# Kernel tuning notes

Hardware: AMD Instinct MI355X
Metric: run time of the kernel (lower is better)

## Reference

```python
import jax, jax.numpy as jnp
import numpy as np

N = 100000      # nodes
F_IN = 512      # input features
H = 128         # hidden
C = 16          # classes
E = 3200000     # edges
K = 10          # propagation hops (lg_k == gg_k == 10)
ALPHA = 0.1


def ppr_temp(K, alpha):
    t = alpha * (1.0 - alpha) ** np.arange(K + 1)
    t[-1] = (1.0 - alpha) ** K
    return jnp.asarray(t, dtype=jnp.float32)


def setup_inputs() -> dict:
    key = jax.random.key(0)
    ks = jax.random.split(key, 8)
    x = jax.random.normal(ks[0], (N, F_IN), dtype=jnp.float32)
    edge_index = jax.random.randint(ks[1], (2, E), 0, N, dtype=jnp.int64)
    # Local branch: kaiming-uniform-ish linears
    W1_l = jax.random.uniform(ks[2], (F_IN, H), jnp.float32, -1.0, 1.0) * np.sqrt(6.0 / F_IN)
    b1_l = jnp.zeros((H,), jnp.float32)
    W2_l = jax.random.uniform(ks[3], (H, C), jnp.float32, -1.0, 1.0) * np.sqrt(6.0 / H)
    b2_l = jnp.zeros((C,), jnp.float32)
    temp_l = ppr_temp(K, ALPHA)
    # Global branch: uniform(-0.1, 0.1) linears
    W1_g = jax.random.uniform(ks[4], (F_IN, H), jnp.float32, -0.1, 0.1)
    b1_g = jnp.zeros((H,), jnp.float32)
    W2_g = jax.random.uniform(ks[5], (H, C), jnp.float32, -0.1, 0.1)
    b2_g = jnp.zeros((C,), jnp.float32)
    temp_g = ppr_temp(K, ALPHA)
    return {"x": x, "edge_index": edge_index,
            "W1_l": W1_l, "b1_l": b1_l, "W2_l": W2_l, "b2_l": b2_l, "temp_l": temp_l,
            "W1_g": W1_g, "b1_g": b1_g, "W2_g": W2_g, "b2_g": b2_g, "temp_g": temp_g}


def gpr_prop(x, edge_index, temp):
    # gcn_norm: add self-loops with weight 1, symmetric normalization
    row = jnp.concatenate([edge_index[0], jnp.arange(N, dtype=edge_index.dtype)])
    col = jnp.concatenate([edge_index[1], jnp.arange(N, dtype=edge_index.dtype)])
    deg = jax.ops.segment_sum(jnp.ones(row.shape[0], x.dtype), col, num_segments=N)
    dis = jnp.where(deg > 0, jax.lax.rsqrt(deg), 0.0).astype(x.dtype)
    norm = dis[row] * dis[col]  # [E+N]

    def step(carry, gamma):
        xc, hid = carry
        # gather-scale-scatter: out[col] += norm * xc[row]
        xn = jax.ops.segment_sum(norm[:, None] * xc[row], col, num_segments=N)
        return (xn, hid + gamma * xn), None

    (_, hidden), _ = jax.lax.scan(step, (x, x * temp[0]), temp[1:])
    return hidden


def gprgnn_branch(x, edge_index, W1, b1, W2, b2, temp):
    h1 = jax.nn.relu(x @ W1 + b1)          # [N, H]
    h2 = h1 @ W2 + b2                      # [N, C]
    h2 = gpr_prop(h2, edge_index, temp)    # K-hop GPR diffusion
    return h1, h2, jax.nn.log_softmax(h2, axis=1)


def reference(x, edge_index, W1_l, b1_l, W2_l, b2_l, temp_l,
              W1_g, b1_g, W2_g, b2_g, temp_g):
    h1_l, h2_l, prob_l = gprgnn_branch(x, edge_index, W1_l, b1_l, W2_l, b2_l, temp_l)
    h1_g, h2_g, prob_g = gprgnn_branch(x, edge_index, W1_g, b1_g, W2_g, b2_g, temp_g)
    return (h1_l, h2_l, prob_l, h1_g, h2_g, prob_g)
```

## Files before the change

### kernel.cpp

```cpp
#include <hip/hip_runtime.h>
#include <stdint.h>

#define F_IN 512
#define HDIM 128
#define CDIM 16
#define KHOPS 10

#define NBMAX 1024
#define CSTR 16
#define CHUNK 8192
#define CH2 32768

typedef __bf16 bf16x8 __attribute__((ext_vector_type(8)));
typedef float f32x4 __attribute__((ext_vector_type(4)));

typedef __attribute__((address_space(3))) unsigned int lds_uint;
typedef const __attribute__((address_space(1))) unsigned int g_uint;

__device__ __forceinline__ void dma16(const void* g, void* l) {
    __builtin_amdgcn_global_load_lds((g_uint*)g, (lds_uint*)l, 16, 0, 0);
}

__device__ __forceinline__ unsigned short f2bf(float f) {
    unsigned int u = __float_as_uint(f);
    u += 0x7FFFu + ((u >> 16) & 1u);
    return (unsigned short)(u >> 16);
}

__device__ __forceinline__ bf16x8 ld_bf8(const unsigned short* p) {
    uint4 u = *reinterpret_cast<const uint4*>(p);
    return __builtin_bit_cast(bf16x8, u);
}


__global__ __launch_bounds__(256) void k_ccount(const int* __restrict__ eidx,
                                                int* __restrict__ ccnt, int E) {
    __shared__ int lh[NBMAX];
    int t = threadIdx.x;
    int base = blockIdx.x * CH2;
    int lim = E - base; if (lim > CH2) lim = CH2;
    for (int i = t; i < NBMAX; i += 256) lh[i] = 0;
    __syncthreads();
    for (int j = t; j < lim; j += 256)
        atomicAdd(&lh[eidx[(size_t)E + base + j] >> 8], 1);
    __syncthreads();
    for (int i = t; i < NBMAX; i += 256) {
        int v = lh[i];
        if (v) atomicAdd(&ccnt[i], v);
    }
}

__global__ void k_cscan(const int* __restrict__ ccnt, int* __restrict__ coffs,
                        int* __restrict__ ccur, int nbuk) {
    __shared__ int sh[256];
    int t = threadIdx.x;
    int i0 = t * 4;
    int v0 = ccnt[i0 + 0], v1 = ccnt[i0 + 1], v2 = ccnt[i0 + 2], v3 = ccnt[i0 + 3];
    int s = v0 + v1 + v2 + v3;
    sh[t] = s;
    __syncthreads();
    for (int d = 1; d < 256; d <<= 1) {
        int x = (t >= d) ? sh[t - d] : 0;
        __syncthreads();
        sh[t] += x;
        __syncthreads();
    }
    int e0 = sh[t] - s;
    int e1 = e0 + v0, e2 = e1 + v1, e3 = e2 + v2;
    coffs[i0 + 0] = e0;
    coffs[i0 + 1] = e1;
    coffs[i0 + 2] = e2;
    coffs[i0 + 3] = e3;
    if (t == 255) coffs[1024] = e3 + v3;
    if (i0 + 0 < nbuk) ccur[(i0 + 0) * CSTR] = e0;
    if (i0 + 1 < nbuk) ccur[(i0 + 1) * CSTR] = e1;
    if (i0 + 2 < nbuk) ccur[(i0 + 2) * CSTR] = e2;
    if (i0 + 3 < nbuk) ccur[(i0 + 3) * CSTR] = e3;
}

__global__ __launch_bounds__(256) void k_part(
    const int* __restrict__ eidx, int* __restrict__ ccur,
    uint2* __restrict__ cedges, int E)
{
    __shared__ int lh[NBMAX];
    __shared__ int loff[NBMAX];
    __shared__ int lcur[NBMAX];
    __shared__ int gbase[NBMAX];
    __shared__ int sh[256];

    int t = threadIdx.x;
    int base = blockIdx.x * CHUNK;
    int lim = E - base; if (lim > CHUNK) lim = CHUNK;

    for (int i = t; i < NBMAX; i += 256) lh[i] = 0;
    __syncthreads();

    for (int j = t; j < lim; j += 256) {
        int c = eidx[(size_t)E + base + j];
        atomicAdd(&lh[c >> 8], 1);
    }
    __syncthreads();

    int i0 = t * 4;
    int v0 = lh[i0 + 0], v1 = lh[i0 + 1], v2 = lh[i0 + 2], v3 = lh[i0 + 3];
    int s = v0 + v1 + v2 + v3;
    sh[t] = s;
    __syncthreads();
    for (int d = 1; d < 256; d <<= 1) {
        int x = (t >= d) ? sh[t - d] : 0;
        __syncthreads();
        sh[t] += x;
        __syncthreads();
    }
    int excl = sh[t] - s;
    loff[i0 + 0] = excl; lcur[i0 + 0] = excl;
    gbase[i0 + 0] = v0 ? atomicAdd(&ccur[(i0 + 0) * CSTR], v0) : 0;
    excl += v0;
    loff[i0 + 1] = excl; lcur[i0 + 1] = excl;
    gbase[i0 + 1] = v1 ? atomicAdd(&ccur[(i0 + 1) * CSTR], v1) : 0;
    excl += v1;
    loff[i0 + 2] = excl; lcur[i0 + 2] = excl;
    gbase[i0 + 2] = v2 ? atomicAdd(&ccur[(i0 + 2) * CSTR], v2) : 0;
    excl += v2;
    loff[i0 + 3] = excl; lcur[i0 + 3] = excl;
    gbase[i0 + 3] = v3 ? atomicAdd(&ccur[(i0 + 3) * CSTR], v3) : 0;
    __syncthreads();

    for (int j = t; j < lim; j += 256) {
        int r = eidx[base + j];
        int c = eidx[(size_t)E + base + j];
        int b = c >> 8;
        int lp = atomicAdd(&lcur[b], 1);
        int gpos = gbase[b] + (lp - loff[b]);
        uint2 u; u.x = (unsigned)r; u.y = (unsigned)c;
        cedges[gpos] = u;
    }
}

__global__ __launch_bounds__(256) void k_fineA(
    const uint2* __restrict__ cedges, const int* __restrict__ coffs,
    int* __restrict__ cnt, float* __restrict__ dis, int* __restrict__ offs, int N)
{
    __shared__ int lh[256];
    __shared__ int sh[256];
    int b = blockIdx.x;
    int t = threadIdx.x;
    int col0 = b << 8;
    int segs = coffs[b];
    int sege = coffs[b + 1];
    lh[t] = 0;
    __syncthreads();
    for (int j = segs + t; j < sege; j += 256)
        atomicAdd(&lh[(int)cedges[j].y - col0], 1);
    __syncthreads();
    int c = lh[t];
    sh[t] = c;
    __syncthreads();
    for (int d = 1; d < 256; d <<= 1) {
        int x = (t >= d) ? sh[t - d] : 0;
        __syncthreads();
        sh[t] += x;
        __syncthreads();
    }
    int excl = sh[t] - c;
    int col = col0 + t;
    if (col < N) {
        cnt[col] = c;
        dis[col] = rsqrtf((float)(c + 1));
        offs[col] = segs + excl;
    }
}

__global__ __launch_bounds__(256) void k_fineB(
    const uint2* __restrict__ cedges, const int* __restrict__ coffs,
    const int* __restrict__ offs, const float* __restrict__ dis,
    uint2* __restrict__ srcnrm, int N)
{
    __shared__ int lcur[256];
    __shared__ float ldis[256];
    int b = blockIdx.x;
    int col0 = b << 8;
    int t = threadIdx.x;
    int col = col0 + t;
    int segs = coffs[b];
    int sege = coffs[b + 1];
    if (col < N) { lcur[t] = offs[col]; ldis[t] = dis[col]; }
    __syncthreads();
    for (int j = segs + t; j < sege; j += 256) {
        uint2 e = cedges[j];
        int li = (int)e.y - col0;
        int pos = atomicAdd(&lcur[li], 1);
        uint2 u;
        u.x = e.x;
        u.y = __float_as_uint(dis[e.x] * ldis[li]);
        srcnrm[pos] = u;
    }
}


__global__ void k_xbf(const float* __restrict__ x, unsigned short* __restrict__ xbf) {
    size_t i = (size_t)blockIdx.x * 2048 + (size_t)threadIdx.x * 8;
    float4 a = *reinterpret_cast<const float4*>(&x[i]);
    float4 b = *reinterpret_cast<const float4*>(&x[i + 4]);
    unsigned short s[8];
    s[0] = f2bf(a.x); s[1] = f2bf(a.y); s[2] = f2bf(a.z); s[3] = f2bf(a.w);
    s[4] = f2bf(b.x); s[5] = f2bf(b.y); s[6] = f2bf(b.z); s[7] = f2bf(b.w);
    *reinterpret_cast<uint4*>(&xbf[i]) = *reinterpret_cast<uint4*>(s);
}


__global__ void k_w1t(const float* __restrict__ W1l, const float* __restrict__ W1g,
                      unsigned short* __restrict__ W1Tl, unsigned short* __restrict__ W1Tg) {
    const float* W1 = blockIdx.y ? W1g : W1l;
    unsigned short* W1T = blockIdx.y ? W1Tg : W1Tl;
    int idx = blockIdx.x * 256 + threadIdx.x;
    int n = idx >> 6;
    int k0 = (idx & 63) * 8;
    unsigned short tmp[8];
    for (int j = 0; j < 8; j++)
        tmp[j] = f2bf(W1[(size_t)(k0 + j) * HDIM + n]);
    *reinterpret_cast<uint4*>(&W1T[(size_t)n * F_IN + k0]) = *reinterpret_cast<uint4*>(tmp);
}


__global__ __launch_bounds__(256, 4) void k_gemm(
    const unsigned short* __restrict__ xbf,
    const unsigned short* __restrict__ W1Tl, const float* __restrict__ b1l,
    const float* __restrict__ W2l, const float* __restrict__ b2l, const float* __restrict__ tl,
    const unsigned short* __restrict__ W1Tg, const float* __restrict__ b1g,
    const float* __restrict__ W2g, const float* __restrict__ b2g, const float* __restrict__ tg,
    float* __restrict__ h1l, float* __restrict__ h1g,
    float* __restrict__ xc0, float* __restrict__ hid, int nNode)
{
    const int br = blockIdx.y;
    const unsigned short* w1t = br ? W1Tg : W1Tl;
    const float* B1 = br ? b1g : b1l;
    const float* W2 = br ? W2g : W2l;
    const float* B2 = br ? b2g : b2l;
    const float* tp = br ? tg : tl;
    float* h1 = br ? h1g : h1l;

    __shared__ __align__(16) unsigned short sm[17408];
    unsigned short* As = sm;
    unsigned short* Bs = sm + 8192;
    unsigned short* Hs = sm;

    const int t = threadIdx.x;
    const int lane = t & 63;
    const int w = t >> 6;
    const int row0 = blockIdx.x * 128;

    f32x4 acc[2][8];
    for (int i = 0; i < 2; i++)
        for (int j = 0; j < 8; j++)
            acc[i][j] = f32x4{0.f, 0.f, 0.f, 0.f};

    const int m16 = lane & 15;
    const int q = lane >> 4;

    for (int k0 = 0; k0 < F_IN; k0 += 64) {
        #pragma unroll
        for (int j = 0; j < 4; j++) {
            int S0 = w * 256 + j * 64;
            int S = S0 + lane;
            int row = S >> 3;
            int cb = (S & 7) ^ (row & 7);
            dma16(&xbf[(size_t)(row0 + row) * F_IN + k0 + cb * 8], &As[(size_t)S0 * 8]);
        }
        #pragma unroll
        for (int j = 0; j < 4; j++) {
            int S0 = w * 256 + j * 64;
            int S = S0 + lane;
            int n = S >> 3;
            int cb = (S & 7) ^ (n & 7);
            dma16(&w1t[(size_t)n * F_IN + k0 + cb * 8], &Bs[(size_t)S0 * 8]);
        }
        __syncthreads();

        #pragma unroll
        for (int ksub = 0; ksub < 2; ksub++) {
            bf16x8 bf[8];
            #pragma unroll
            for (int ns = 0; ns < 8; ns++) {
                int n = ns * 16 + m16;
                int slot = n * 8 + ((ksub * 4 + q) ^ (n & 7));
                bf[ns] = ld_bf8(&Bs[slot * 8]);
            }
            bf16x8 af[2];
            #pragma unroll
            for (int ms = 0; ms < 2; ms++) {
                int row = w * 32 + ms * 16 + m16;
                int slot = row * 8 + ((ksub * 4 + q) ^ (row & 7));
                af[ms] = ld_bf8(&As[slot * 8]);
            }
            #pragma unroll
            for (int ns = 0; ns < 8; ns++)
                #pragma unroll
                for (int ms = 0; ms < 2; ms++)
                    acc[ms][ns] = __builtin_amdgcn_mfma_f32_16x16x32_bf16(af[ms], bf[ns], acc[ms][ns], 0, 0, 0);
        }
        __syncthreads();
    }

    #pragma unroll
    for (int ms = 0; ms < 2; ms++) {
        #pragma unroll
        for (int ns = 0; ns < 8; ns++) {
            int n = ns * 16 + m16;
            float bias = B1[n];
            #pragma unroll
            for (int r = 0; r < 4; r++) {
                int m = w * 32 + ms * 16 + q * 4 + r;
                float v = acc[ms][ns][r] + bias;
                v = v > 0.f ? v : 0.f;
                Hs[m * 136 + n] = f2bf(v);
                int node = row0 + m;
                if (node < nNode) h1[(size_t)node * HDIM + n] = v;
            }
        }
    }
    __syncthreads();

    {
        float t0 = tp[0];
        float bias = B2[m16];
        #pragma unroll
        for (int mi = 0; mi < 2; mi++) {
            int mt = w * 2 + mi;
            f32x4 acc2 = f32x4{bias, bias, bias, bias};
            #pragma unroll
            for (int kb = 0; kb < 4; kb++) {
                bf16x8 hf = ld_bf8(&Hs[(mt * 16 + m16) * 136 + kb * 32 + q * 8]);
                unsigned short wtmp[8];
                #pragma unroll
                for (int j = 0; j < 8; j++)
                    wtmp[j] = f2bf(W2[(size_t)(kb * 32 + q * 8 + j) * CDIM + m16]);
                bf16x8 wf = ld_bf8(wtmp);
                acc2 = __builtin_amdgcn_mfma_f32_16x16x32_bf16(hf, wf, acc2, 0, 0, 0);
            }
            #pragma unroll
            for (int r = 0; r < 4; r++) {
                int node = row0 + mt * 16 + q * 4 + r;
                if (node < nNode) {
                    size_t idx = (size_t)node * 32 + (size_t)br * 16 + m16;
                    xc0[idx] = acc2[r];
                    hid[idx] = t0 * acc2[r];
                }
            }
        }
    }
}


__global__ __launch_bounds__(256) void k_hop(
    const float* __restrict__ xin, float* __restrict__ xout,
    float* __restrict__ hid, const uint2* __restrict__ srcnrm,
    const int* __restrict__ offs, const int* __restrict__ cnt,
    const float* __restrict__ dis,
    const float* __restrict__ tl, const float* __restrict__ tg,
    int hop, int N)
{
    int t = threadIdx.x;
    int v = blockIdx.x * 32 + (t >> 3);
    int c4 = (t & 7) * 4;
    if (v >= N) return;
    int off = offs[v];
    int m = cnt[v];
    float d = dis[v];
    size_t vbase = (size_t)v * 32 + c4;
    float4 xv = *reinterpret_cast<const float4*>(xin + vbase);
    float dd = d * d;
    float4 acc = make_float4(dd * xv.x, dd * xv.y, dd * xv.z, dd * xv.w);
    const uint2* ep = srcnrm + off;
    int i = 0;
    for (; i + 8 <= m; i += 8) {
        uint2 u[8];
        #pragma unroll
        for (int j = 0; j < 8; j++) u[j] = ep[i + j];
        float4 xs[8];
        #pragma unroll
        for (int j = 0; j < 8; j++)
            xs[j] = *reinterpret_cast<const float4*>(xin + (size_t)u[j].x * 32 + c4);
        #pragma unroll
        for (int j = 0; j < 8; j++) {
            float nrm = __uint_as_float(u[j].y);
            acc.x = fmaf(nrm, xs[j].x, acc.x);
            acc.y = fmaf(nrm, xs[j].y, acc.y);
            acc.z = fmaf(nrm, xs[j].z, acc.z);
            acc.w = fmaf(nrm, xs[j].w, acc.w);
        }
    }
    for (; i < m; i++) {
        uint2 u = ep[i];
        float nrm = __uint_as_float(u.y);
        float4 xs = *reinterpret_cast<const float4*>(xin + (size_t)u.x * 32 + c4);
        acc.x = fmaf(nrm, xs.x, acc.x);
        acc.y = fmaf(nrm, xs.y, acc.y);
        acc.z = fmaf(nrm, xs.z, acc.z);
        acc.w = fmaf(nrm, xs.w, acc.w);
    }
    *reinterpret_cast<float4*>(xout + vbase) = acc;
    float gamma = (c4 < 16 ? tl : tg)[hop];
    float4 h = *reinterpret_cast<const float4*>(hid + vbase);
    h.x = fmaf(gamma, acc.x, h.x);
    h.y = fmaf(gamma, acc.y, h.y);
    h.z = fmaf(gamma, acc.z, h.z);
    h.w = fmaf(gamma, acc.w, h.w);
    *reinterpret_cast<float4*>(hid + vbase) = h;
}


__global__ void k_final(const float* __restrict__ hid,
                        float* __restrict__ h2l, float* __restrict__ pl,
                        float* __restrict__ h2g, float* __restrict__ pg, int N)
{
    int t = threadIdx.x;
    int v = blockIdx.x * 128 + (t >> 1);
    int br = t & 1;
    if (v >= N) return;
    float xv[16];
    const float* src = &hid[(size_t)v * 32 + (size_t)br * 16];
    for (int j = 0; j < 16; j += 4)
        *reinterpret_cast<float4*>(&xv[j]) = *reinterpret_cast<const float4*>(&src[j]);
    float mx = xv[0];
    for (int j = 1; j < 16; j++) mx = fmaxf(mx, xv[j]);
    float s = 0.f;
    for (int j = 0; j < 16; j++) s += __expf(xv[j] - mx);
    float lse = mx + __logf(s);
    float* h2 = br ? h2g : h2l;
    float* pp = br ? pg : pl;
    for (int j = 0; j < 16; j++) {
        h2[(size_t)v * 16 + j] = xv[j];
        pp[(size_t)v * 16 + j] = xv[j] - lse;
    }
}


extern "C" void kernel_launch(void* const* d_in, const int* in_sizes, int n_in,
                              void* d_out, int out_size, void* d_ws, size_t ws_size,
                              hipStream_t stream)
{
    const float* x   = (const float*)d_in[0];
    const int*   eidx= (const int*)d_in[1];
    const float* W1l = (const float*)d_in[2];
    const float* b1l = (const float*)d_in[3];
    const float* W2l = (const float*)d_in[4];
    const float* b2l = (const float*)d_in[5];
    const float* tl  = (const float*)d_in[6];
    const float* W1g = (const float*)d_in[7];
    const float* b1g = (const float*)d_in[8];
    const float* W2g = (const float*)d_in[9];
    const float* b2g = (const float*)d_in[10];
    const float* tg  = (const float*)d_in[11];

    const int N = in_sizes[0] / F_IN;
    const int E = in_sizes[1] / 2;

    float* out = (float*)d_out;
    float* h1l = out;
    float* h2l = h1l + (size_t)N * HDIM;
    float* pl  = h2l + (size_t)N * CDIM;
    float* h1g = pl  + (size_t)N * CDIM;
    float* h2g = h1g + (size_t)N * HDIM;
    float* pg  = h2g + (size_t)N * CDIM;

    char* ws = (char*)d_ws;
    auto alloc = [&](size_t bytes) -> char* {
        char* p = ws;
        ws += (bytes + 1023) & ~(size_t)1023;
        return p;
    };
    int*   cnt      = (int*)alloc((size_t)N * 4);
    int*   offs     = (int*)alloc((size_t)N * 4);
    int*   ccnt     = (int*)alloc((size_t)(NBMAX + 1) * 4);
    int*   coffs    = (int*)alloc((size_t)(NBMAX + 1) * 4);
    int*   ccur     = (int*)alloc((size_t)NBMAX * CSTR * 4);
    float* dis      = (float*)alloc((size_t)N * 4);
    uint2* srcnrm   = (uint2*)alloc((size_t)E * 8);
    float* xcA      = (float*)alloc((size_t)N * 32 * 4);
    float* xcB      = (float*)alloc((size_t)N * 32 * 4);
    float* hid      = (float*)alloc((size_t)N * 32 * 4);
    unsigned short* W1Tl = (unsigned short*)alloc((size_t)HDIM * F_IN * 2);
    unsigned short* W1Tg = (unsigned short*)alloc((size_t)HDIM * F_IN * 2);
    unsigned short* xbf  = (unsigned short*)alloc((size_t)(N + 256) * F_IN * 2);
    uint2* cedges = (uint2*)xbf;

    hipMemsetAsync(ccnt, 0, (size_t)(NBMAX + 1) * 4, stream);

    int nbuk = (N + 255) / 256;

    k_ccount<<<(E + CH2 - 1) / CH2, 256, 0, stream>>>(eidx, ccnt, E);
    k_cscan<<<1, 256, 0, stream>>>(ccnt, coffs, ccur, nbuk);
    k_part<<<(E + CHUNK - 1) / CHUNK, 256, 0, stream>>>(eidx, ccur, cedges, E);
    k_fineA<<<nbuk, 256, 0, stream>>>(cedges, coffs, cnt, dis, offs, N);
    k_fineB<<<nbuk, 256, 0, stream>>>(cedges, coffs, offs, dis, srcnrm, N);

    k_xbf<<<(int)(((size_t)N * F_IN) / 2048), 256, 0, stream>>>(x, xbf);
    dim3 gw(32, 2);
    k_w1t<<<gw, 256, 0, stream>>>(W1l, W1g, W1Tl, W1Tg);

    dim3 gg((N + 127) / 128, 2);
    k_gemm<<<gg, 256, 0, stream>>>(xbf, W1Tl, b1l, W2l, b2l, tl,
                                   W1Tg, b1g, W2g, b2g, tg,
                                   h1l, h1g, xcA, hid, N);

    int gh = (N + 31) / 32;
    float* a = xcA;
    float* b = xcB;
    for (int k = 1; k <= KHOPS; k++) {
        k_hop<<<gh, 256, 0, stream>>>(a, b, hid, srcnrm, offs, cnt, dis, tl, tg, k, N);
        float* tmp = a; a = b; b = tmp;
    }
    k_final<<<(N + 127) / 128, 256, 0, stream>>>(hid, h2l, pl, h2g, pg, N);
}
```

Before: 1.189 ms.

## Fuse K propagation hops and log-softmax into one persistent kernel with grid barriers

Replaces the ten per-hop launches and the final log-softmax kernel with one persistent kernel of 1024 blocks. Each thread keeps its node slices, the hidden accumulator and the degree data in registers across hops, and a global atomic barrier separates the hops. The edge norm is factored into source and destination scaling, so the edge list shrinks from 8 bytes to 4 bytes per edge and the hidden state is never written to memory. The risks are the correctness of the spin barrier, which needs all blocks co-resident (1024 blocks at 4 per CU), and less latency hiding, since each thread walks up to four node slices one after another.

```diff
diff --git a/kernel.cpp b/kernel.cpp
--- a/kernel.cpp
+++ b/kernel.cpp
@@ -10,6 +10,9 @@
 #define CSTR 16
 #define CHUNK 8192
 #define CH2 32768
+
+#define PROP_BLOCKS 1024
+#define MAXIT 4
 
 typedef __bf16 bf16x8 __attribute__((ext_vector_type(8)));
 typedef float f32x4 __attribute__((ext_vector_type(4)));
@@ -173,27 +176,22 @@
 
 __global__ __launch_bounds__(256) void k_fineB(
     const uint2* __restrict__ cedges, const int* __restrict__ coffs,
-    const int* __restrict__ offs, const float* __restrict__ dis,
-    uint2* __restrict__ srcnrm, int N)
+    const int* __restrict__ offs, int* __restrict__ srcs, int N)
 {
     __shared__ int lcur[256];
-    __shared__ float ldis[256];
     int b = blockIdx.x;
     int col0 = b << 8;
     int t = threadIdx.x;
     int col = col0 + t;
     int segs = coffs[b];
     int sege = coffs[b + 1];
-    if (col < N) { lcur[t] = offs[col]; ldis[t] = dis[col]; }
+    if (col < N) lcur[t] = offs[col];
     __syncthreads();
     for (int j = segs + t; j < sege; j += 256) {
         uint2 e = cedges[j];
         int li = (int)e.y - col0;
         int pos = atomicAdd(&lcur[li], 1);
-        uint2 u;
-        u.x = e.x;
-        u.y = __float_as_uint(dis[e.x] * ldis[li]);
-        srcnrm[pos] = u;
+        srcs[pos] = (int)e.x;
     }
 }
 
@@ -226,18 +224,17 @@
 __global__ __launch_bounds__(256, 4) void k_gemm(
     const unsigned short* __restrict__ xbf,
     const unsigned short* __restrict__ W1Tl, const float* __restrict__ b1l,
-    const float* __restrict__ W2l, const float* __restrict__ b2l, const float* __restrict__ tl,
+    const float* __restrict__ W2l, const float* __restrict__ b2l,
     const unsigned short* __restrict__ W1Tg, const float* __restrict__ b1g,
-    const float* __restrict__ W2g, const float* __restrict__ b2g, const float* __restrict__ tg,
+    const float* __restrict__ W2g, const float* __restrict__ b2g,
     float* __restrict__ h1l, float* __restrict__ h1g,
-    float* __restrict__ xc0, float* __restrict__ hid, int nNode)
+    float* __restrict__ xc0, int nNode)
 {
     const int br = blockIdx.y;
     const unsigned short* w1t = br ? W1Tg : W1Tl;
     const float* B1 = br ? b1g : b1l;
     const float* W2 = br ? W2g : W2l;
     const float* B2 = br ? b2g : b2l;
-    const float* tp = br ? tg : tl;
     float* h1 = br ? h1g : h1l;
 
     __shared__ __align__(16) unsigned short sm[17408];
@@ -322,7 +319,6 @@
     __syncthreads();
 
     {
-        float t0 = tp[0];
         float bias = B2[m16];
         #pragma unroll
         for (int mi = 0; mi < 2; mi++) {
@@ -344,7 +340,6 @@
                 if (node < nNode) {
                     size_t idx = (size_t)node * 32 + (size_t)br * 16 + m16;
                     xc0[idx] = acc2[r];
-                    hid[idx] = t0 * acc2[r];
                 }
             }
         }
@@ -352,86 +347,128 @@
 }
 
 
-__global__ __launch_bounds__(256) void k_hop(
-    const float* __restrict__ xin, float* __restrict__ xout,
-    float* __restrict__ hid, const uint2* __restrict__ srcnrm,
-    const int* __restrict__ offs, const int* __restrict__ cnt,
-    const float* __restrict__ dis,
+__device__ __forceinline__ void gbar(unsigned int* bar, unsigned int tgt) {
+    __threadfence();
+    __syncthreads();
+    if (threadIdx.x == 0) {
+        atomicAdd(bar, 1u);
+        while (atomicAdd(bar, 0u) < tgt) __builtin_amdgcn_s_sleep(2);
+    }
+    __syncthreads();
+    __threadfence();
+}
+
+__global__ __launch_bounds__(256, 4) void k_prop(
+    const float* __restrict__ x0,
+    float* __restrict__ yA, float* __restrict__ yB,
+    const int* __restrict__ srcs, const int* __restrict__ offs,
+    const int* __restrict__ cnt, const float* __restrict__ dis,
     const float* __restrict__ tl, const float* __restrict__ tg,
-    int hop, int N)
+    float* __restrict__ h2l, float* __restrict__ pl,
+    float* __restrict__ h2g, float* __restrict__ pg,
+    unsigned int* __restrict__ bar, int N)
 {
-    int t = threadIdx.x;
-    int v = blockIdx.x * 32 + (t >> 3);
-    int c4 = (t & 7) * 4;
-    if (v >= N) return;
-    int off = offs[v];
-    int m = cnt[v];
-    float d = dis[v];
-    size_t vbase = (size_t)v * 32 + c4;
-    float4 xv = *reinterpret_cast<const float4*>(xin + vbase);
-    float dd = d * d;
-    float4 acc = make_float4(dd * xv.x, dd * xv.y, dd * xv.z, dd * xv.w);
-    const uint2* ep = srcnrm + off;
-    int i = 0;
-    for (; i + 8 <= m; i += 8) {
-        uint2 u[8];
+    const int T = gridDim.x * 256;
+    const int gtid = blockIdx.x * 256 + threadIdx.x;
+    const int NP = N * 8;
+    const int slice = gtid & 7;
+    const int c4 = slice * 4;
+    const float* tp = slice < 4 ? tl : tg;
+
+    float4 cur[MAXIT], hid[MAXIT];
+    int off[MAXIT], deg[MAXIT];
+    float dv[MAXIT];
+
+    const float t0 = tp[0];
+    #pragma unroll
+    for (int it = 0; it < MAXIT; ++it) {
+        int p = it * T + gtid;
+        if (p < NP) {
+            int v = p >> 3;
+            off[it] = offs[v];
+            deg[it] = cnt[v];
+            float d = dis[v];
+            dv[it] = d;
+            float4 xv = *reinterpret_cast<const float4*>(x0 + (size_t)p * 4);
+            cur[it] = make_float4(d * xv.x, d * xv.y, d * xv.z, d * xv.w);
+            hid[it] = make_float4(t0 * xv.x, t0 * xv.y, t0 * xv.z, t0 * xv.w);
+            *reinterpret_cast<float4*>(yA + (size_t)p * 4) = cur[it];
+        } else {
+            off[it] = 0; deg[it] = 0; dv[it] = 0.f;
+            cur[it] = make_float4(0.f, 0.f, 0.f, 0.f);
+            hid[it] = make_float4(0.f, 0.f, 0.f, 0.f);
+        }
+    }
+
+    gbar(bar, gridDim.x);
+
+    const float* yin = yA;
+    float* yout = yB;
+    for (int k = 1; k <= KHOPS; ++k) {
+        float gma = tp[k];
         #pragma unroll
-        for (int j = 0; j < 8; j++) u[j] = ep[i + j];
-        float4 xs[8];
-        #pragma unroll
-        for (int j = 0; j < 8; j++)
-            xs[j] = *reinterpret_cast<const float4*>(xin + (size_t)u[j].x * 32 + c4);
-        #pragma unroll
-        for (int j = 0; j < 8; j++) {
-            float nrm = __uint_as_float(u[j].y);
-            acc.x = fmaf(nrm, xs[j].x, acc.x);
-            acc.y = fmaf(nrm, xs[j].y, acc.y);
-            acc.z = fmaf(nrm, xs[j].z, acc.z);
-            acc.w = fmaf(nrm, xs[j].w, acc.w);
-        }
-    }
-    for (; i < m; i++) {
-        uint2 u = ep[i];
-        float nrm = __uint_as_float(u.y);
-        float4 xs = *reinterpret_cast<const float4*>(xin + (size_t)u.x * 32 + c4);
-        acc.x = fmaf(nrm, xs.x, acc.x);
-        acc.y = fmaf(nrm, xs.y, acc.y);
-        acc.z = fmaf(nrm, xs.z, acc.z);
-        acc.w = fmaf(nrm, xs.w, acc.w);
-    }
-    *reinterpret_cast<float4*>(xout + vbase) = acc;
-    float gamma = (c4 < 16 ? tl : tg)[hop];
-    float4 h = *reinterpret_cast<const float4*>(hid + vbase);
-    h.x = fmaf(gamma, acc.x, h.x);
-    h.y = fmaf(gamma, acc.y, h.y);
-    h.z = fmaf(gamma, acc.z, h.z);
-    h.w = fmaf(gamma, acc.w, h.w);
-    *reinterpret_cast<float4*>(hid + vbase) = h;
-}
-
-
-__global__ void k_final(const float* __restrict__ hid,
-                        float* __restrict__ h2l, float* __restrict__ pl,
-                        float* __restrict__ h2g, float* __restrict__ pg, int N)
-{
-    int t = threadIdx.x;
-    int v = blockIdx.x * 128 + (t >> 1);
-    int br = t & 1;
-    if (v >= N) return;
-    float xv[16];
-    const float* src = &hid[(size_t)v * 32 + (size_t)br * 16];
-    for (int j = 0; j < 16; j += 4)
-        *reinterpret_cast<float4*>(&xv[j]) = *reinterpret_cast<const float4*>(&src[j]);
-    float mx = xv[0];
-    for (int j = 1; j < 16; j++) mx = fmaxf(mx, xv[j]);
-    float s = 0.f;
-    for (int j = 0; j < 16; j++) s += __expf(xv[j] - mx);
-    float lse = mx + __logf(s);
-    float* h2 = br ? h2g : h2l;
-    float* pp = br ? pg : pl;
-    for (int j = 0; j < 16; j++) {
-        h2[(size_t)v * 16 + j] = xv[j];
-        pp[(size_t)v * 16 + j] = xv[j] - lse;
+        for (int it = 0; it < MAXIT; ++it) {
+            int p = it * T + gtid;
+            if (p >= NP) continue;
+            const int* ep = srcs + off[it];
+            int m = deg[it];
+            float4 acc = cur[it];
+            int i = 0;
+            for (; i + 8 <= m; i += 8) {
+                int u[8];
+                #pragma unroll
+                for (int j = 0; j < 8; ++j) u[j] = ep[i + j];
+                float4 xs[8];
+                #pragma unroll
+                for (int j = 0; j < 8; ++j)
+                    xs[j] = *reinterpret_cast<const float4*>(yin + (size_t)u[j] * 32 + c4);
+                #pragma unroll
+                for (int j = 0; j < 8; ++j) {
+                    acc.x += xs[j].x; acc.y += xs[j].y;
+                    acc.z += xs[j].z; acc.w += xs[j].w;
+                }
+            }
+            for (; i < m; ++i) {
+                float4 xs = *reinterpret_cast<const float4*>(yin + (size_t)ep[i] * 32 + c4);
+                acc.x += xs.x; acc.y += xs.y; acc.z += xs.z; acc.w += xs.w;
+            }
+            float d = dv[it];
+            float4 xn = make_float4(d * acc.x, d * acc.y, d * acc.z, d * acc.w);
+            hid[it].x = fmaf(gma, xn.x, hid[it].x);
+            hid[it].y = fmaf(gma, xn.y, hid[it].y);
+            hid[it].z = fmaf(gma, xn.z, hid[it].z);
+            hid[it].w = fmaf(gma, xn.w, hid[it].w);
+            cur[it] = make_float4(d * xn.x, d * xn.y, d * xn.z, d * xn.w);
+            if (k < KHOPS)
+                *reinterpret_cast<float4*>(yout + (size_t)p * 4) = cur[it];
+        }
+        if (k < KHOPS) {
+            gbar(bar, (unsigned)(k + 1) * gridDim.x);
+            const float* tin = yin; yin = yout; yout = (float*)tin;
+        }
+    }
+
+    #pragma unroll
+    for (int it = 0; it < MAXIT; ++it) {
+        int p = it * T + gtid;
+        float4 hv = hid[it];
+        float mloc = fmaxf(fmaxf(hv.x, hv.y), fmaxf(hv.z, hv.w));
+        mloc = fmaxf(mloc, __shfl_xor(mloc, 1));
+        mloc = fmaxf(mloc, __shfl_xor(mloc, 2));
+        float sl = __expf(hv.x - mloc) + __expf(hv.y - mloc) +
+                   __expf(hv.z - mloc) + __expf(hv.w - mloc);
+        sl += __shfl_xor(sl, 1);
+        sl += __shfl_xor(sl, 2);
+        float lse = mloc + __logf(sl);
+        if (p < NP) {
+            int v = p >> 3;
+            int r = (slice & 3) * 4;
+            float* h2 = slice < 4 ? h2l : h2g;
+            float* pp = slice < 4 ? pl : pg;
+            *reinterpret_cast<float4*>(h2 + (size_t)v * 16 + r) = hv;
+            float4 po = make_float4(hv.x - lse, hv.y - lse, hv.z - lse, hv.w - lse);
+            *reinterpret_cast<float4*>(pp + (size_t)v * 16 + r) = po;
+        }
     }
 }
 
@@ -475,17 +512,19 @@
     int*   ccnt     = (int*)alloc((size_t)(NBMAX + 1) * 4);
     int*   coffs    = (int*)alloc((size_t)(NBMAX + 1) * 4);
     int*   ccur     = (int*)alloc((size_t)NBMAX * CSTR * 4);
+    unsigned int* bar = (unsigned int*)alloc(1024);
     float* dis      = (float*)alloc((size_t)N * 4);
-    uint2* srcnrm   = (uint2*)alloc((size_t)E * 8);
+    int*   srcs     = (int*)alloc((size_t)E * 4);
     float* xcA      = (float*)alloc((size_t)N * 32 * 4);
-    float* xcB      = (float*)alloc((size_t)N * 32 * 4);
-    float* hid      = (float*)alloc((size_t)N * 32 * 4);
+    float* yA       = (float*)alloc((size_t)N * 32 * 4);
+    float* yB       = (float*)alloc((size_t)N * 32 * 4);
     unsigned short* W1Tl = (unsigned short*)alloc((size_t)HDIM * F_IN * 2);
     unsigned short* W1Tg = (unsigned short*)alloc((size_t)HDIM * F_IN * 2);
     unsigned short* xbf  = (unsigned short*)alloc((size_t)(N + 256) * F_IN * 2);
     uint2* cedges = (uint2*)xbf;
 
     hipMemsetAsync(ccnt, 0, (size_t)(NBMAX + 1) * 4, stream);
+    hipMemsetAsync(bar, 0, 1024, stream);
 
     int nbuk = (N + 255) / 256;
 
@@ -493,23 +532,17 @@
     k_cscan<<<1, 256, 0, stream>>>(ccnt, coffs, ccur, nbuk);
     k_part<<<(E + CHUNK - 1) / CHUNK, 256, 0, stream>>>(eidx, ccur, cedges, E);
     k_fineA<<<nbuk, 256, 0, stream>>>(cedges, coffs, cnt, dis, offs, N);
-    k_fineB<<<nbuk, 256, 0, stream>>>(cedges, coffs, offs, dis, srcnrm, N);
+    k_fineB<<<nbuk, 256, 0, stream>>>(cedges, coffs, offs, srcs, N);
 
     k_xbf<<<(int)(((size_t)N * F_IN) / 2048), 256, 0, stream>>>(x, xbf);
     dim3 gw(32, 2);
     k_w1t<<<gw, 256, 0, stream>>>(W1l, W1g, W1Tl, W1Tg);
 
     dim3 gg((N + 127) / 128, 2);
-    k_gemm<<<gg, 256, 0, stream>>>(xbf, W1Tl, b1l, W2l, b2l, tl,
-                                   W1Tg, b1g, W2g, b2g, tg,
-                                   h1l, h1g, xcA, hid, N);
-
-    int gh = (N + 31) / 32;
-    float* a = xcA;
-    float* b = xcB;
-    for (int k = 1; k <= KHOPS; k++) {
-        k_hop<<<gh, 256, 0, stream>>>(a, b, hid, srcnrm, offs, cnt, dis, tl, tg, k, N);
-        float* tmp = a; a = b; b = tmp;
-    }
-    k_final<<<(N + 127) / 128, 256, 0, stream>>>(hid, h2l, pl, h2g, pg, N);
-}
+    k_gemm<<<gg, 256, 0, stream>>>(xbf, W1Tl, b1l, W2l, b2l,
+                                   W1Tg, b1g, W2g, b2g,
+                                   h1l, h1g, xcA, N);
+
+    k_prop<<<PROP_BLOCKS, 256, 0, stream>>>(xcA, yA, yB, srcs, offs, cnt, dis,
+                                            tl, tg, h2l, pl, h2g, pg, bar, N);
+}
```

Result: slower. 3.429 ms (+188.5%).

## Fold symmetric norm into prescaled features and split propagation into channel passes

Applied to the files above, without the earlier changes.

Propagation now stores y = D^{-1/2} x, so each hop becomes a plain sum of gathered neighbour rows, scaled by dis[v] on output. This drops the per-edge norm weight and halves the edge array to a single int per edge. Features move to a pass-major layout (8 passes of float4 per node), with one thread per node per pass, so each gather reads a 16-byte row from a compact 1.6MB slab that fits in cache, instead of eight threads sharing a 128-byte row. The trade-off is more index reads, since each edge's source index is now loaded once per pass (eight times per hop).

```diff
diff --git a/kernel.cpp b/kernel.cpp
--- a/kernel.cpp
+++ b/kernel.cpp
@@ -173,27 +173,22 @@
 
 __global__ __launch_bounds__(256) void k_fineB(
     const uint2* __restrict__ cedges, const int* __restrict__ coffs,
-    const int* __restrict__ offs, const float* __restrict__ dis,
-    uint2* __restrict__ srcnrm, int N)
+    const int* __restrict__ offs, int* __restrict__ srcs, int N)
 {
     __shared__ int lcur[256];
-    __shared__ float ldis[256];
     int b = blockIdx.x;
     int col0 = b << 8;
     int t = threadIdx.x;
     int col = col0 + t;
     int segs = coffs[b];
     int sege = coffs[b + 1];
-    if (col < N) { lcur[t] = offs[col]; ldis[t] = dis[col]; }
+    if (col < N) lcur[t] = offs[col];
     __syncthreads();
     for (int j = segs + t; j < sege; j += 256) {
         uint2 e = cedges[j];
         int li = (int)e.y - col0;
         int pos = atomicAdd(&lcur[li], 1);
-        uint2 u;
-        u.x = e.x;
-        u.y = __float_as_uint(dis[e.x] * ldis[li]);
-        srcnrm[pos] = u;
+        srcs[pos] = (int)e.x;
     }
 }
 
@@ -229,8 +224,9 @@
     const float* __restrict__ W2l, const float* __restrict__ b2l, const float* __restrict__ tl,
     const unsigned short* __restrict__ W1Tg, const float* __restrict__ b1g,
     const float* __restrict__ W2g, const float* __restrict__ b2g, const float* __restrict__ tg,
+    const float* __restrict__ dis,
     float* __restrict__ h1l, float* __restrict__ h1g,
-    float* __restrict__ xc0, float* __restrict__ hid, int nNode)
+    float* __restrict__ y0, float* __restrict__ hidb, int nNode)
 {
     const int br = blockIdx.y;
     const unsigned short* w1t = br ? W1Tg : W1Tl;
@@ -324,6 +320,8 @@
     {
         float t0 = tp[0];
         float bias = B2[m16];
+        int pass = br * 4 + (m16 >> 2);
+        int slot = m16 & 3;
         #pragma unroll
         for (int mi = 0; mi < 2; mi++) {
             int mt = w * 2 + mi;
@@ -342,9 +340,10 @@
             for (int r = 0; r < 4; r++) {
                 int node = row0 + mt * 16 + q * 4 + r;
                 if (node < nNode) {
-                    size_t idx = (size_t)node * 32 + (size_t)br * 16 + m16;
-                    xc0[idx] = acc2[r];
-                    hid[idx] = t0 * acc2[r];
+                    size_t idx = ((size_t)pass * nNode + node) * 4 + slot;
+                    float val = acc2[r];
+                    y0[idx] = dis[node] * val;
+                    hidb[idx] = t0 * val;
                 }
             }
         }
@@ -352,65 +351,58 @@
 }
 
 
-__global__ __launch_bounds__(256) void k_hop(
-    const float* __restrict__ xin, float* __restrict__ xout,
-    float* __restrict__ hid, const uint2* __restrict__ srcnrm,
+__global__ __launch_bounds__(256) void k_hop2(
+    const float* __restrict__ yin, float* __restrict__ yout,
+    float* __restrict__ hidb, const int* __restrict__ srcs,
     const int* __restrict__ offs, const int* __restrict__ cnt,
     const float* __restrict__ dis,
     const float* __restrict__ tl, const float* __restrict__ tg,
-    int hop, int N)
-{
-    int t = threadIdx.x;
-    int v = blockIdx.x * 32 + (t >> 3);
-    int c4 = (t & 7) * 4;
+    int hop, int N, int last)
+{
+    int pass = blockIdx.x & 7;
+    int v = (blockIdx.x >> 3) * 256 + threadIdx.x;
     if (v >= N) return;
+    const float4* yin_s = reinterpret_cast<const float4*>(yin) + (size_t)pass * N;
+    float4* yout_s = reinterpret_cast<float4*>(yout) + (size_t)pass * N;
+    float4* hid_s = reinterpret_cast<float4*>(hidb) + (size_t)pass * N;
+
     int off = offs[v];
     int m = cnt[v];
     float d = dis[v];
-    size_t vbase = (size_t)v * 32 + c4;
-    float4 xv = *reinterpret_cast<const float4*>(xin + vbase);
-    float dd = d * d;
-    float4 acc = make_float4(dd * xv.x, dd * xv.y, dd * xv.z, dd * xv.w);
-    const uint2* ep = srcnrm + off;
+    float4 acc = yin_s[v];
+    const int* ep = srcs + off;
     int i = 0;
     for (; i + 8 <= m; i += 8) {
-        uint2 u[8];
-        #pragma unroll
-        for (int j = 0; j < 8; j++) u[j] = ep[i + j];
+        int u[8];
+        #pragma unroll
+        for (int j = 0; j < 8; ++j) u[j] = ep[i + j];
         float4 xs[8];
         #pragma unroll
-        for (int j = 0; j < 8; j++)
-            xs[j] = *reinterpret_cast<const float4*>(xin + (size_t)u[j].x * 32 + c4);
-        #pragma unroll
-        for (int j = 0; j < 8; j++) {
-            float nrm = __uint_as_float(u[j].y);
-            acc.x = fmaf(nrm, xs[j].x, acc.x);
-            acc.y = fmaf(nrm, xs[j].y, acc.y);
-            acc.z = fmaf(nrm, xs[j].z, acc.z);
-            acc.w = fmaf(nrm, xs[j].w, acc.w);
+        for (int j = 0; j < 8; ++j) xs[j] = yin_s[u[j]];
+        #pragma unroll
+        for (int j = 0; j < 8; ++j) {
+            acc.x += xs[j].x; acc.y += xs[j].y;
+            acc.z += xs[j].z; acc.w += xs[j].w;
         }
     }
-    for (; i < m; i++) {
-        uint2 u = ep[i];
-        float nrm = __uint_as_float(u.y);
-        float4 xs = *reinterpret_cast<const float4*>(xin + (size_t)u.x * 32 + c4);
-        acc.x = fmaf(nrm, xs.x, acc.x);
-        acc.y = fmaf(nrm, xs.y, acc.y);
-        acc.z = fmaf(nrm, xs.z, acc.z);
-        acc.w = fmaf(nrm, xs.w, acc.w);
-    }
-    *reinterpret_cast<float4*>(xout + vbase) = acc;
-    float gamma = (c4 < 16 ? tl : tg)[hop];
-    float4 h = *reinterpret_cast<const float4*>(hid + vbase);
-    h.x = fmaf(gamma, acc.x, h.x);
-    h.y = fmaf(gamma, acc.y, h.y);
-    h.z = fmaf(gamma, acc.z, h.z);
-    h.w = fmaf(gamma, acc.w, h.w);
-    *reinterpret_cast<float4*>(hid + vbase) = h;
-}
-
-
-__global__ void k_final(const float* __restrict__ hid,
+    for (; i < m; ++i) {
+        float4 xs = yin_s[ep[i]];
+        acc.x += xs.x; acc.y += xs.y; acc.z += xs.z; acc.w += xs.w;
+    }
+    float4 xn = make_float4(d * acc.x, d * acc.y, d * acc.z, d * acc.w);
+    float gamma = (pass < 4 ? tl : tg)[hop];
+    float4 h = hid_s[v];
+    h.x = fmaf(gamma, xn.x, h.x);
+    h.y = fmaf(gamma, xn.y, h.y);
+    h.z = fmaf(gamma, xn.z, h.z);
+    h.w = fmaf(gamma, xn.w, h.w);
+    hid_s[v] = h;
+    if (!last)
+        yout_s[v] = make_float4(d * xn.x, d * xn.y, d * xn.z, d * xn.w);
+}
+
+
+__global__ void k_final(const float* __restrict__ hidb,
                         float* __restrict__ h2l, float* __restrict__ pl,
                         float* __restrict__ h2g, float* __restrict__ pg, int N)
 {
@@ -419,9 +411,10 @@
     int br = t & 1;
     if (v >= N) return;
     float xv[16];
-    const float* src = &hid[(size_t)v * 32 + (size_t)br * 16];
-    for (int j = 0; j < 16; j += 4)
-        *reinterpret_cast<float4*>(&xv[j]) = *reinterpret_cast<const float4*>(&src[j]);
+    #pragma unroll
+    for (int cb = 0; cb < 4; cb++)
+        *reinterpret_cast<float4*>(&xv[cb * 4]) =
+            *reinterpret_cast<const float4*>(hidb + ((size_t)(br * 4 + cb) * N + v) * 4);
     float mx = xv[0];
     for (int j = 1; j < 16; j++) mx = fmaxf(mx, xv[j]);
     float s = 0.f;
@@ -476,10 +469,10 @@
     int*   coffs    = (int*)alloc((size_t)(NBMAX + 1) * 4);
     int*   ccur     = (int*)alloc((size_t)NBMAX * CSTR * 4);
     float* dis      = (float*)alloc((size_t)N * 4);
-    uint2* srcnrm   = (uint2*)alloc((size_t)E * 8);
-    float* xcA      = (float*)alloc((size_t)N * 32 * 4);
-    float* xcB      = (float*)alloc((size_t)N * 32 * 4);
-    float* hid      = (float*)alloc((size_t)N * 32 * 4);
+    int*   srcs     = (int*)alloc((size_t)E * 4);
+    float* yA       = (float*)alloc((size_t)N * 32 * 4);
+    float* yB       = (float*)alloc((size_t)N * 32 * 4);
+    float* hidb     = (float*)alloc((size_t)N * 32 * 4);
     unsigned short* W1Tl = (unsigned short*)alloc((size_t)HDIM * F_IN * 2);
     unsigned short* W1Tg = (unsigned short*)alloc((size_t)HDIM * F_IN * 2);
     unsigned short* xbf  = (unsigned short*)alloc((size_t)(N + 256) * F_IN * 2);
@@ -493,7 +486,7 @@
     k_cscan<<<1, 256, 0, stream>>>(ccnt, coffs, ccur, nbuk);
     k_part<<<(E + CHUNK - 1) / CHUNK, 256, 0, stream>>>(eidx, ccur, cedges, E);
     k_fineA<<<nbuk, 256, 0, stream>>>(cedges, coffs, cnt, dis, offs, N);
-    k_fineB<<<nbuk, 256, 0, stream>>>(cedges, coffs, offs, dis, srcnrm, N);
+    k_fineB<<<nbuk, 256, 0, stream>>>(cedges, coffs, offs, srcs, N);
 
     k_xbf<<<(int)(((size_t)N * F_IN) / 2048), 256, 0, stream>>>(x, xbf);
     dim3 gw(32, 2);
@@ -501,15 +494,16 @@
 
     dim3 gg((N + 127) / 128, 2);
     k_gemm<<<gg, 256, 0, stream>>>(xbf, W1Tl, b1l, W2l, b2l, tl,
-                                   W1Tg, b1g, W2g, b2g, tg,
-                                   h1l, h1g, xcA, hid, N);
-
-    int gh = (N + 31) / 32;
-    float* a = xcA;
-    float* b = xcB;
+                                   W1Tg, b1g, W2g, b2g, tg, dis,
+                                   h1l, h1g, yA, hidb, N);
+
+    int gh = ((N + 255) / 256) * 8;
+    float* a = yA;
+    float* b = yB;
     for (int k = 1; k <= KHOPS; k++) {
-        k_hop<<<gh, 256, 0, stream>>>(a, b, hid, srcnrm, offs, cnt, dis, tl, tg, k, N);
+        k_hop2<<<gh, 256, 0, stream>>>(a, b, hidb, srcs, offs, cnt, dis,
+                                       tl, tg, k, N, k == KHOPS);
         float* tmp = a; a = b; b = tmp;
     }
-    k_final<<<(N + 127) / 128, 256, 0, stream>>>(hid, h2l, pl, h2g, pg, N);
-}
+    k_final<<<(N + 127) / 128, 256, 0, stream>>>(hidb, h2l, pl, h2g, pg, N);
+}
```

After: 1.952 ms. 1.64x slower.
